# Kernel optimization log

Measured on AMD Instinct MI355X. Metric: run time of the kernel, lower is better.

## Reference

```python
import jax, jax.numpy as jnp
import numpy as np

FEATURE_BITWIDTH = 8
INPUT_ZERO_POINT = 0
OUTPUT_ZERO_POINT = 0
INPUT_SCALE = 0.02
OUTPUT_SCALE = 0.1
STRIDE = (1, 1)
PAD = (1, 1)  # (padH, padW)
DILATION = (1, 1)

QMIN = -(1 << (FEATURE_BITWIDTH - 1))          # -128
QMAX = (1 << (FEATURE_BITWIDTH - 1)) - 1       # 127


def setup_inputs() -> dict:
    key = jax.random.key(0)
    k1, k2, k3, k4 = jax.random.split(key, 4)
    N, Cin, H, W = 32, 128, 56, 56
    Cout, kH, kW = 256, 3, 3
    x = jax.random.randint(k1, (N, Cin, H, W), -128, 128, dtype=jnp.int32).astype(jnp.int8)
    weight = jax.random.randint(k2, (Cout, Cin, kH, kW), -128, 128, dtype=jnp.int32).astype(jnp.int8)
    bias = jax.random.randint(k3, (Cout,), -1000, 1000, dtype=jnp.int32)
    weight_scale = jax.random.uniform(k4, (Cout,), dtype=jnp.float32, minval=0.001, maxval=0.01)
    return {"x": x, "weight": weight, "bias": bias, "weight_scale": weight_scale}


def reference(x, weight, bias, weight_scale):
    # Pad spatial dims with the input zero point (asymmetric quant padding).
    padH, padW = PAD
    xp = jnp.pad(x.astype(jnp.int32),
                 ((0, 0), (0, 0), (padH, padH), (padW, padW)),
                 constant_values=INPUT_ZERO_POINT)
    # Integer conv accumulation in int32 (matches CPU path exactly).
    acc = jax.lax.conv_general_dilated(
        xp, weight.astype(jnp.int32),
        window_strides=STRIDE, padding='VALID',
        rhs_dilation=DILATION,
        dimension_numbers=('NCHW', 'OIHW', 'NCHW'))  # [N, Cout, Ho, Wo] int32
    acc = acc + bias[None, :, None, None]
    # Fused dequant -> requant epilogue with per-output-channel scale.
    scale = (INPUT_SCALE * weight_scale / OUTPUT_SCALE)[None, :, None, None]
    out = acc.astype(jnp.float32) * scale + OUTPUT_ZERO_POINT
    out = jnp.clip(jnp.round(out), QMIN, QMAX).astype(jnp.int8)
    return out
```

## Files before the change

kernel.cpp:

```cpp
#include <hip/hip_runtime.h>

#define N_      32
#define CIN     128
#define HW_     56
#define COUT    256
#define HP      58
#define SP_     (HW_*HW_)
#define M_      (N_*SP_)
#define ROWB    7424
#define CHB     928
#define XP_BYTES (N_*HP*ROWB)
#define WP_BYTES (9*COUT*CIN)
#define TAPB    32768
#define NWG     ((M_/256)*(COUT/64))
#define PERX    (NWG/8)
#define RX_BLKS (N_*HP)
#define RW_BLKS (WP_BYTES/4/256)

typedef int int4v  __attribute__((ext_vector_type(4)));
typedef int int16v __attribute__((ext_vector_type(16)));

__global__ __launch_bounds__(256) void repack(const int* __restrict__ x32,
                                              const int* __restrict__ w32,
                                              char* __restrict__ xp,
                                              char* __restrict__ wp) {
    int b = blockIdx.x;
    if (b < RX_BLKS) {
        __shared__ char s8[CIN * HW_];
        int n = b / HP;
        int hp = b - n * HP;
        int h = hp - 1;
        bool live = (h >= 0) && (h < HW_);
        if (live) {
            const int* src = x32 + ((size_t)(n * CIN)) * SP_ + h * HW_;
            for (int i = threadIdx.x; i < CIN * HW_; i += 256) {
                int c = i / HW_, w = i - c * HW_;
                s8[i] = (char)src[c * SP_ + w];
            }
        }
        __syncthreads();
        int* dst = (int*)(xp + (size_t)b * ROWB);
        for (int i = threadIdx.x; i < 8 * 232; i += 256) {
            int chunk = i / 232, r = i - chunk * 232;
            int wp_ = r >> 2, sub = r & 3;
            int w = wp_ - 1;
            int v = 0;
            if (live && w >= 0 && w < HW_) {
                int c0 = chunk * 16 + sub * 4;
                int v0 = (unsigned char)s8[(c0 + 0) * HW_ + w];
                int v1 = (unsigned char)s8[(c0 + 1) * HW_ + w];
                int v2 = (unsigned char)s8[(c0 + 2) * HW_ + w];
                int v3 = (unsigned char)s8[(c0 + 3) * HW_ + w];
                v = v0 | (v1 << 8) | (v2 << 16) | (v3 << 24);
            }
            dst[i] = v;
        }
    } else {
        int i = (b - RX_BLKS) * 256 + threadIdx.x;
        int tap   = i >> 13;
        int r     = i & 8191;
        int panel = r >> 11;
        int r2    = r & 2047;
        int half  = r2 >> 10;
        int kc    = (r2 >> 8) & 3;
        int lh    = (r2 >> 7) & 1;
        int co32  = (r2 >> 2) & 31;
        int db    = r2 & 3;
        int co = panel * 64 + half * 32 + co32;
        int c0 = kc * 32 + lh * 16 + db * 4;
        const int* s = w32 + co * (CIN * 9) + c0 * 9 + tap;
        int v0 = s[0]  & 0xff;
        int v1 = s[9]  & 0xff;
        int v2 = s[18] & 0xff;
        int v3 = s[27] & 0xff;
        ((int*)wp)[i] = v0 | (v1 << 8) | (v2 << 16) | (v3 << 24);
    }
}

__global__ __launch_bounds__(256, 2) void conv_mfma(const char* __restrict__ xp,
                                                    const char* __restrict__ wp,
                                                    const int*  __restrict__ bias,
                                                    const float* __restrict__ wsc,
                                                    int* __restrict__ out) {
    __shared__ char Bs[9 * 8192];
    const int tid  = threadIdx.x;
    const int wave = tid >> 6, lane = tid & 63;
    const int l31 = lane & 31, lh = lane >> 5;

    int bid = blockIdx.x;
    int w_  = (bid & 7) * PERX + (bid >> 3);
    const int co0    = (w_ & 3) << 6;
    const int m_base = (w_ >> 2) << 8;

    const char* aptrT[2];
    int tb[2];
#pragma unroll
    for (int mf = 0; mf < 2; ++mf) {
        tb[mf] = m_base + wave * 64 + mf * 32;
        int row = tb[mf] + l31;
        int n  = row / SP_;
        int sp = row - n * SP_;
        int ho = sp / HW_;
        int wo = sp - ho * HW_;
        aptrT[mf] = xp + (size_t)(n * HP + ho) * ROWB + lh * CHB + wo * 16;
    }

    const char* wpb = wp + (co0 >> 6) * 8192;

    int16v acc[2][2] = {};

    for (int i = wave; i < 72; i += 4) {
        int p = (i << 10) + (lane << 4);
        const char* src = wpb + (p >> 13) * TAPB + (p & 8191);
        __builtin_amdgcn_global_load_lds(
            (const __attribute__((address_space(1))) void*)src,
            (__attribute__((address_space(3))) void*)&Bs[i << 10], 16, 0, 0);
    }

    auto aload = [&](int4v a[2][4], int tap) {
        int kh = tap / 3, kw = tap - kh * 3;
        int aoff = kh * ROWB + kw * 16;
#pragma unroll
        for (int kc = 0; kc < 4; ++kc) {
            a[0][kc] = *(const int4v*)(aptrT[0] + aoff + kc * (2 * CHB));
            a[1][kc] = *(const int4v*)(aptrT[1] + aoff + kc * (2 * CHB));
        }
    };

    auto ctap = [&](const int4v a[2][4], int tap) {
        int bbase = (tap << 13) + (lane << 4);
        __builtin_amdgcn_s_setprio(1);
        int4v b0[4], b1[4];
#pragma unroll
        for (int kc = 0; kc < 4; ++kc) {
            b0[kc] = *(const int4v*)&Bs[bbase + kc * 1024];
            b1[kc] = *(const int4v*)&Bs[bbase + 4096 + kc * 1024];
        }
#pragma unroll
        for (int kc = 0; kc < 4; ++kc) {
            acc[0][0] = __builtin_amdgcn_mfma_i32_32x32x32_i8(a[0][kc], b0[kc], acc[0][0], 0, 0, 0);
            acc[1][0] = __builtin_amdgcn_mfma_i32_32x32x32_i8(a[1][kc], b0[kc], acc[1][0], 0, 0, 0);
            acc[0][1] = __builtin_amdgcn_mfma_i32_32x32x32_i8(a[0][kc], b1[kc], acc[0][1], 0, 0, 0);
            acc[1][1] = __builtin_amdgcn_mfma_i32_32x32x32_i8(a[1][kc], b1[kc], acc[1][1], 0, 0, 0);
        }
        __builtin_amdgcn_s_setprio(0);
    };

    int4v aA[2][4], aB[2][4], aC[2][4];

    aload(aA, 0);
    aload(aB, 1);
    __syncthreads();

    aload(aC, 2); ctap(aA, 0);
    aload(aA, 3); ctap(aB, 1);
    aload(aB, 4); ctap(aC, 2);
    aload(aC, 5); ctap(aA, 3);
    aload(aA, 6); ctap(aB, 4);
    aload(aB, 7); ctap(aC, 5);
    aload(aC, 8); ctap(aA, 6);
    ctap(aB, 7);
    ctap(aC, 8);

#pragma unroll
    for (int mf = 0; mf < 2; ++mf) {
        int nu  = tb[mf] / SP_;
        int sp0 = tb[mf] - nu * SP_;
#pragma unroll
        for (int nf = 0; nf < 2; ++nf) {
            int co = co0 + nf * 32 + l31;
            float s = (0.02f * wsc[co]) / 0.1f;
            int bs = bias[co];
            int* ob = out + ((size_t)(nu * COUT + co)) * SP_ + sp0 + (lh << 2);
#pragma unroll
            for (int g = 0; g < 4; ++g) {
                int4v qv;
#pragma unroll
                for (int r = 0; r < 4; ++r) {
                    float v = (float)(acc[mf][nf][g * 4 + r] + bs) * s;
                    int q = (int)rintf(v);
                    qv[r] = q < -128 ? -128 : (q > 127 ? 127 : q);
                }
                *(int4v*)(ob + g * 8) = qv;
            }
        }
    }
}

extern "C" void kernel_launch(void* const* d_in, const int* in_sizes, int n_in,
                              void* d_out, int out_size, void* d_ws, size_t ws_size,
                              hipStream_t stream) {
    const int*   x32  = (const int*)d_in[0];
    const int*   w32  = (const int*)d_in[1];
    const int*   bias = (const int*)d_in[2];
    const float* wsc  = (const float*)d_in[3];

    char* xp = (char*)d_ws;
    char* wp = xp + XP_BYTES;

    repack<<<dim3(RX_BLKS + RW_BLKS), 256, 0, stream>>>(x32, w32, xp, wp);
    conv_mfma<<<dim3(NWG), 256, 0, stream>>>(xp, wp, bias, wsc, (int*)d_out);
}
```

Measured before the change: 66.35 us.

## Shrink conv tile to 32 output channels per block for higher occupancy

Halves the per-block output-channel tile from 64 to 32, doubling the grid, and repacks the weight panels to match the new 32-channel layout. LDS for the weights drops to 36 KB, accumulators drop to two tiles per wave, and the A-operand triple buffer becomes a double buffer. Launch bounds rise to 3 blocks per CU. The goal is more resident waves to hide latency. The cost is that each loaded activation tile is reused for only half as many output channels, doubling global/L2 traffic for activations, and each tap issues fewer MFMAs to cover load latency.

```diff
diff --git a/kernel.cpp b/kernel.cpp
--- a/kernel.cpp
+++ b/kernel.cpp
@@ -12,7 +12,7 @@
 #define XP_BYTES (N_*HP*ROWB)
 #define WP_BYTES (9*COUT*CIN)
 #define TAPB    32768
-#define NWG     ((M_/256)*(COUT/64))
+#define NWG     ((M_/256)*(COUT/32))
 #define PERX    (NWG/8)
 #define RX_BLKS (N_*HP)
 #define RW_BLKS (WP_BYTES/4/256)
@@ -59,14 +59,13 @@
         int i = (b - RX_BLKS) * 256 + threadIdx.x;
         int tap   = i >> 13;
         int r     = i & 8191;
-        int panel = r >> 11;
-        int r2    = r & 2047;
-        int half  = r2 >> 10;
-        int kc    = (r2 >> 8) & 3;
+        int panel = r >> 10;
+        int r2    = r & 1023;
+        int kc    = r2 >> 8;
         int lh    = (r2 >> 7) & 1;
         int co32  = (r2 >> 2) & 31;
         int db    = r2 & 3;
-        int co = panel * 64 + half * 32 + co32;
+        int co = panel * 32 + co32;
         int c0 = kc * 32 + lh * 16 + db * 4;
         const int* s = w32 + co * (CIN * 9) + c0 * 9 + tap;
         int v0 = s[0]  & 0xff;
@@ -77,20 +76,20 @@
     }
 }
 
-__global__ __launch_bounds__(256, 2) void conv_mfma(const char* __restrict__ xp,
+__global__ __launch_bounds__(256, 3) void conv_mfma(const char* __restrict__ xp,
                                                     const char* __restrict__ wp,
                                                     const int*  __restrict__ bias,
                                                     const float* __restrict__ wsc,
                                                     int* __restrict__ out) {
-    __shared__ char Bs[9 * 8192];
+    __shared__ char Bs[9 * 4096];
     const int tid  = threadIdx.x;
     const int wave = tid >> 6, lane = tid & 63;
     const int l31 = lane & 31, lh = lane >> 5;
 
     int bid = blockIdx.x;
     int w_  = (bid & 7) * PERX + (bid >> 3);
-    const int co0    = (w_ & 3) << 6;
-    const int m_base = (w_ >> 2) << 8;
+    const int co0    = (w_ & 7) << 5;
+    const int m_base = (w_ >> 3) << 8;
 
     const char* aptrT[2];
     int tb[2];
@@ -105,13 +104,13 @@
         aptrT[mf] = xp + (size_t)(n * HP + ho) * ROWB + lh * CHB + wo * 16;
     }
 
-    const char* wpb = wp + (co0 >> 6) * 8192;
+    const char* wpb = wp + (co0 >> 5) * 4096;
 
-    int16v acc[2][2] = {};
+    int16v acc[2] = {};
 
-    for (int i = wave; i < 72; i += 4) {
+    for (int i = wave; i < 36; i += 4) {
         int p = (i << 10) + (lane << 4);
-        const char* src = wpb + (p >> 13) * TAPB + (p & 8191);
+        const char* src = wpb + (p >> 12) * TAPB + (p & 4095);
         __builtin_amdgcn_global_load_lds(
             (const __attribute__((address_space(1))) void*)src,
             (__attribute__((address_space(3))) void*)&Bs[i << 10], 16, 0, 0);
@@ -128,61 +127,53 @@
     };
 
     auto ctap = [&](const int4v a[2][4], int tap) {
-        int bbase = (tap << 13) + (lane << 4);
+        int bbase = (tap << 12) + (lane << 4);
         __builtin_amdgcn_s_setprio(1);
-        int4v b0[4], b1[4];
+        int4v b0[4];
+#pragma unroll
+        for (int kc = 0; kc < 4; ++kc)
+            b0[kc] = *(const int4v*)&Bs[bbase + kc * 1024];
 #pragma unroll
         for (int kc = 0; kc < 4; ++kc) {
-            b0[kc] = *(const int4v*)&Bs[bbase + kc * 1024];
-            b1[kc] = *(const int4v*)&Bs[bbase + 4096 + kc * 1024];
-        }
-#pragma unroll
-        for (int kc = 0; kc < 4; ++kc) {
-            acc[0][0] = __builtin_amdgcn_mfma_i32_32x32x32_i8(a[0][kc], b0[kc], acc[0][0], 0, 0, 0);
-            acc[1][0] = __builtin_amdgcn_mfma_i32_32x32x32_i8(a[1][kc], b0[kc], acc[1][0], 0, 0, 0);
-            acc[0][1] = __builtin_amdgcn_mfma_i32_32x32x32_i8(a[0][kc], b1[kc], acc[0][1], 0, 0, 0);
-            acc[1][1] = __builtin_amdgcn_mfma_i32_32x32x32_i8(a[1][kc], b1[kc], acc[1][1], 0, 0, 0);
+            acc[0] = __builtin_amdgcn_mfma_i32_32x32x32_i8(a[0][kc], b0[kc], acc[0], 0, 0, 0);
+            acc[1] = __builtin_amdgcn_mfma_i32_32x32x32_i8(a[1][kc], b0[kc], acc[1], 0, 0, 0);
         }
         __builtin_amdgcn_s_setprio(0);
     };
 
-    int4v aA[2][4], aB[2][4], aC[2][4];
+    int4v aA[2][4], aB[2][4];
 
     aload(aA, 0);
-    aload(aB, 1);
     __syncthreads();
 
-    aload(aC, 2); ctap(aA, 0);
-    aload(aA, 3); ctap(aB, 1);
-    aload(aB, 4); ctap(aC, 2);
-    aload(aC, 5); ctap(aA, 3);
-    aload(aA, 6); ctap(aB, 4);
-    aload(aB, 7); ctap(aC, 5);
-    aload(aC, 8); ctap(aA, 6);
-    ctap(aB, 7);
-    ctap(aC, 8);
+    aload(aB, 1); ctap(aA, 0);
+    aload(aA, 2); ctap(aB, 1);
+    aload(aB, 3); ctap(aA, 2);
+    aload(aA, 4); ctap(aB, 3);
+    aload(aB, 5); ctap(aA, 4);
+    aload(aA, 6); ctap(aB, 5);
+    aload(aB, 7); ctap(aA, 6);
+    aload(aA, 8); ctap(aB, 7);
+    ctap(aA, 8);
 
 #pragma unroll
     for (int mf = 0; mf < 2; ++mf) {
         int nu  = tb[mf] / SP_;
         int sp0 = tb[mf] - nu * SP_;
+        int co = co0 + l31;
+        float s = (0.02f * wsc[co]) / 0.1f;
+        int bs = bias[co];
+        int* ob = out + ((size_t)(nu * COUT + co)) * SP_ + sp0 + (lh << 2);
 #pragma unroll
-        for (int nf = 0; nf < 2; ++nf) {
-            int co = co0 + nf * 32 + l31;
-            float s = (0.02f * wsc[co]) / 0.1f;
-            int bs = bias[co];
-            int* ob = out + ((size_t)(nu * COUT + co)) * SP_ + sp0 + (lh << 2);
+        for (int g = 0; g < 4; ++g) {
+            int4v qv;
 #pragma unroll
-            for (int g = 0; g < 4; ++g) {
-                int4v qv;
-#pragma unroll
-                for (int r = 0; r < 4; ++r) {
-                    float v = (float)(acc[mf][nf][g * 4 + r] + bs) * s;
-                    int q = (int)rintf(v);
-                    qv[r] = q < -128 ? -128 : (q > 127 ? 127 : q);
-                }
-                *(int4v*)(ob + g * 8) = qv;
+            for (int r = 0; r < 4; ++r) {
+                float v = (float)(acc[mf][g * 4 + r] + bs) * s;
+                int q = (int)rintf(v);
+                qv[r] = q < -128 ? -128 : (q > 127 ? 127 : q);
             }
+            *(int4v*)(ob + g * 8) = qv;
         }
     }
 }
```

After: 82.90 us. 1.25x slower.
